# Kernel tuning notes

Hardware: AMD Instinct MI355X
Metric: run time of the kernel (lower is better)

## Reference

```python
import jax, jax.numpy as jnp
import numpy as np

GAMMA = 1.0
BIG = 1e10  # finite stand-in for +inf boundary; exp(-BIG) underflows to exactly 0 (grad-safe)


def setup_inputs() -> dict:
    key = jax.random.key(0)
    k1, k2 = jax.random.split(key)
    B, L, C = 64, 1024, 64
    x = jax.random.normal(k1, (B, L, C), dtype=jnp.float32)
    y = jax.random.normal(k2, (B, L, C), dtype=jnp.float32)
    return {"x": x, "y": y}


def _soft_dtw(x, y, gamma=GAMMA):
    B, L, C = x.shape
    # squared-euclidean pairwise cost, scaled by 1/gamma (matches torch code)
    x2 = jnp.sum(x * x, axis=-1)[:, :, None]            # [B,L,1]
    y2 = jnp.sum(y * y, axis=-1)[:, None, :]            # [B,1,L]
    D = (x2 + y2 - 2.0 * jnp.einsum('blc,bmc->blm', x, y)) / gamma  # [B,L,L]

    # Anti-diagonal wavefront DP over the (L+2)x(L+2) R matrix.
    # r_d[i] holds R[i, d-i] for the diagonal i+j=d, i in 0..L+1.
    n = L + 2
    ii = jnp.arange(n)
    i_idx = jnp.clip(ii - 1, 0, L - 1)
    r_prev2 = jnp.full((B, n), BIG, dtype=x.dtype).at[:, 0].set(0.0)  # diag d=0: R[0,0]=0
    r_prev1 = jnp.full((B, n), BIG, dtype=x.dtype)                    # diag d=1: all boundary
    big_col = jnp.full((B, 1), BIG, dtype=x.dtype)

    def step(carry, d):
        rp2, rp1 = carry
        jj = d - ii
        valid = (ii >= 1) & (ii <= L) & (jj >= 1) & (jj <= L)
        j_idx = jnp.clip(jj - 1, 0, L - 1)
        d_vals = D[:, i_idx, j_idx]                                   # [B,n] cost along diagonal
        r_diag = jnp.concatenate([big_col, rp2[:, :-1]], axis=1)      # R[i-1, j-1]
        r_up   = jnp.concatenate([big_col, rp1[:, :-1]], axis=1)      # R[i-1, j]
        r_left = rp1                                                  # R[i,   j-1]
        z = jnp.stack([-r_diag, -r_up, -r_left], axis=-1)             # [B,n,3]
        zmax = jnp.max(z, axis=-1)
        softmin = -(jnp.log(jnp.sum(jnp.exp(z - zmax[..., None]), axis=-1)) + zmax)
        new = jnp.where(valid[None, :], d_vals + softmin, BIG)
        return (rp1, new), None

    (_, r_last), _ = jax.lax.scan(step, (r_prev2, r_prev1), jnp.arange(2, 2 * L + 1))
    # last diagonal is d=2L; R[L,L] sits at index i=L
    return r_last[:, L] * gamma


def reference(x, y):
    return _soft_dtw(x, y)
```

## Files before the change

### kernel.cpp

```cpp
#include <hip/hip_runtime.h>


typedef unsigned short ushort_t;
typedef __attribute__((ext_vector_type(8))) short short8;
typedef __attribute__((ext_vector_type(4))) float f32x4;
typedef __attribute__((ext_vector_type(4))) unsigned short ushort4v;

constexpr int B_ = 64, L_ = 1024, C_ = 64;
constexpr int DSTR = 130;
constexpr int HBSTR = 1280;

#define BIGV 1e10f
#define INV_LN2 1.44269504088896340736f
#define LN2F 0.69314718055994530942f
#define DPP_WAVE_SHL1 0x130
#define DPP_WAVE_SHR1 0x138

static __device__ __forceinline__ ushort_t f2bf(float f) {
  unsigned u = __builtin_bit_cast(unsigned, f);
  unsigned r = (u + 0x7fffu + ((u >> 16) & 1u)) >> 16;
  return (ushort_t)r;
}
static __device__ __forceinline__ float exp2_(float x) {
  float r; asm("v_exp_f32 %0, %1" : "=v"(r) : "v"(x)); return r;
}
static __device__ __forceinline__ float log2_(float x) {
  float r; asm("v_log_f32 %0, %1" : "=v"(r) : "v"(x)); return r;
}
static __device__ __forceinline__ unsigned cvt_pk_bf16(float lo, float hi) {
  unsigned r; asm("v_cvt_pk_bf16_f32 %0, %1, %2" : "=v"(r) : "v"(lo), "v"(hi)); return r;
}
static __device__ __forceinline__ float dpp_shr1(float old, float src) {
  return __builtin_bit_cast(float, __builtin_amdgcn_update_dpp(
      __builtin_bit_cast(int, old), __builtin_bit_cast(int, src),
      DPP_WAVE_SHR1, 0xF, 0xF, false));
}
static __device__ __forceinline__ float dpp_shl1(float v) {
  return __builtin_bit_cast(float, __builtin_amdgcn_update_dpp(
      __builtin_bit_cast(int, v), __builtin_bit_cast(int, v),
      DPP_WAVE_SHL1, 0xF, 0xF, false));
}

__global__ __launch_bounds__(256) void prep_kernel(
    const float* __restrict__ x, const float* __restrict__ y,
    ushort_t* __restrict__ xb, ushort_t* __restrict__ yb,
    float* __restrict__ x2, float* __restrict__ y2, int* __restrict__ flagsG)
{
  if (blockIdx.x == 0 && threadIdx.x < 192) flagsG[threadIdx.x] = 0;
  const int lane = threadIdx.x & 63;
  const int sub = lane >> 4;
  const int cg  = lane & 15;
  const int wv = (blockIdx.x * blockDim.x + threadIdx.x) >> 6;
  const int nw = (gridDim.x * blockDim.x) >> 6;
  const int totalGroups = (2 * B_ * L_) >> 2;
  for (int g = wv; g < totalGroups; g += nw) {
    int r = g * 4 + sub;
    const float* src; ushort_t* dst; float* nrm;
    if (r < B_ * L_) { src = x; dst = xb; nrm = x2; }
    else             { r -= B_ * L_; src = y; dst = yb; nrm = y2; }
    const float4 v = *(const float4*)(src + (size_t)r * C_ + cg * 4);
    ushort4v p;
    p.x = f2bf(v.x); p.y = f2bf(v.y); p.z = f2bf(v.z); p.w = f2bf(v.w);
    *(ushort4v*)(dst + (size_t)r * C_ + cg * 4) = p;
    float s = v.x*v.x + v.y*v.y + v.z*v.z + v.w*v.w;
    s += __shfl_xor(s, 1); s += __shfl_xor(s, 2);
    s += __shfl_xor(s, 4); s += __shfl_xor(s, 8);
    if (cg == 0) nrm[r] = s * INV_LN2;
  }
}

template<int HDST, bool FIRST>
static __device__ __forceinline__ void dp_chunk(
    const int t, const int lane, float& cur, float& dgp, float hvv,
    const float zsel, const ushort_t* __restrict__ DtwLane,
    float* __restrict__ HbDst, float* __restrict__ HXB)
{
  const unsigned* pw = (const unsigned*)(DtwLane + ((t << 6) & 127));
  const int cb = (t << 6) - 63;
  unsigned a0 = pw[0], a1 = pw[1], b0 = pw[2], b1 = pw[3];

  auto step = [&](unsigned dw, int k, int u) -> float {
    float dv = __builtin_bit_cast(float, (k & 1) ? (dw & 0xffff0000u) : (dw << 16));
    float up = dpp_shr1(hvv, cur);
    float dg = dgp, lf = cur;
    if constexpr (FIRST) {
      bool at0 = (u == lane);
      dg = at0 ? zsel : dg;
      lf = at0 ? BIGV : lf;
    }
    float mn = fminf(fminf(up, dg), lf);
    float e = exp2_(mn - up) + exp2_(mn - dg) + exp2_(mn - lf);
    float nv = (dv + mn) - log2_(e);
    dgp = up;
    hvv = dpp_shl1(hvv);
    if constexpr (FIRST) { if (u >= lane) cur = nv; }
    else cur = nv;
    return nv;
  };
  auto flush4 = [&](int c0, float v0, float v1, float v2, float v3) {
    if constexpr (HDST == 0) {
      if (lane == 63) { HbDst[c0] = v0; HbDst[c0+1] = v1; HbDst[c0+2] = v2; HbDst[c0+3] = v3; }
    } else if constexpr (HDST == 1) {
      if (lane == 63) { HXB[c0] = v0; HXB[c0+1] = v1; HXB[c0+2] = v2; HXB[c0+3] = v3; }
    }
  };

  #pragma unroll 1
  for (int g = 0; g < 8; ++g) {
    const int u0 = g * 8;
    unsigned n0 = 0, n1 = 0, n2 = 0, n3 = 0;
    if (g < 7) {
      n0 = pw[u0/2 + 4]; n1 = pw[u0/2 + 5]; n2 = pw[u0/2 + 6]; n3 = pw[u0/2 + 7];
    }
    float v0 = step(a0, 0, u0 + 0);
    float v1 = step(a0, 1, u0 + 1);
    float v2 = step(a1, 0, u0 + 2);
    float v3 = step(a1, 1, u0 + 3);
    if constexpr (!FIRST) flush4(cb + u0, v0, v1, v2, v3);
    float v4 = step(b0, 0, u0 + 4);
    float v5 = step(b0, 1, u0 + 5);
    float v6 = step(b1, 0, u0 + 6);
    float v7 = step(b1, 1, u0 + 7);
    if constexpr (!FIRST) flush4(cb + u0 + 4, v4, v5, v6, v7);
    a0 = n0; a1 = n1; b0 = n2; b1 = n3;
    (void)v0; (void)v1; (void)v2; (void)v3; (void)v4; (void)v5; (void)v6; (void)v7;
  }
  if constexpr (FIRST) {
    if constexpr (HDST == 0) { if (lane == 63) HbDst[0] = cur; }
    else if constexpr (HDST == 1) { if (lane == 63) HXB[0] = cur; }
  }
}

template<int HDST>
static __device__ __forceinline__ void dp_tail(
    const int lane, float& cur, float& dgp,
    const ushort_t* __restrict__ DtwLane,
    float* __restrict__ HbDst, float* __restrict__ HXB)
{
  const unsigned* pw = (const unsigned*)(DtwLane);
  #pragma unroll 1
  for (int g = 0; g < 8; ++g) {
    unsigned w0 = pw[g*4], w1 = pw[g*4+1], w2 = pw[g*4+2], w3 = pw[g*4+3];
    #pragma unroll
    for (int k = 0; k < 8; ++k) {
      const int u = g * 8 + k;
      unsigned dw = (k < 2) ? w0 : (k < 4) ? w1 : (k < 6) ? w2 : w3;
      float dv = __builtin_bit_cast(float, (k & 1) ? (dw & 0xffff0000u) : (dw << 16));
      float up = dpp_shr1(BIGV, cur);
      float dg = dgp, lf = cur;
      float mn = fminf(fminf(up, dg), lf);
      float e = exp2_(mn - up) + exp2_(mn - dg) + exp2_(mn - lf);
      float nv = (dv + mn) - log2_(e);
      dgp = up;
      if (u < lane) {
        cur = nv;
        if constexpr (HDST == 0) { if (lane == 63) HbDst[961 + u] = nv; }
        else if constexpr (HDST == 1) { if (lane == 63) HXB[961 + u] = nv; }
      }
    }
  }
}

static __device__ __forceinline__ void spin_lds(int* f, int v) {
  int k = 0;
  while (__hip_atomic_load(f, __ATOMIC_ACQUIRE, __HIP_MEMORY_SCOPE_WORKGROUP) < v) {
    __builtin_amdgcn_s_sleep(1);
    if (++k > (1 << 26)) break;
  }
}
static __device__ __forceinline__ void spin_glb(int* f, int v) {
  int k = 0;
  while (__hip_atomic_load(f, __ATOMIC_ACQUIRE, __HIP_MEMORY_SCOPE_AGENT) < v) {
    __builtin_amdgcn_s_sleep(8);
    if (++k > (1 << 26)) break;
  }
}

template<int HSRC, int HDST>
static __device__ __forceinline__ void run_band(
    const ushort_t* __restrict__ xbB, const ushort_t* __restrict__ ybB,
    const float* __restrict__ x2B, const float* __restrict__ y2B,
    const float* __restrict__ HXin, float* __restrict__ HXout,
    int* __restrict__ fGin, int* __restrict__ fGout,
    ushort_t* __restrict__ Dtw, const float* __restrict__ HbSrc,
    float* __restrict__ HbDst, int* __restrict__ cin, int* __restrict__ cout,
    const int lane, const int W, float* __restrict__ outp)
{
  const int m = lane & 15, q = lane >> 4;
  const int i0 = W * 64;

  short8 af[4][2];
  #pragma unroll
  for (int mt = 0; mt < 4; ++mt)
    #pragma unroll
    for (int ks = 0; ks < 2; ++ks)
      af[mt][ks] = *(const short8*)(xbB + (size_t)(i0 + mt * 16 + m) * C_ + ks * 32 + q * 8);
  f32x4 x2q[4];
  #pragma unroll
  for (int mt = 0; mt < 4; ++mt) x2q[mt] = *(const f32x4*)(x2B + i0 + mt * 16 + q * 4);

  short8 bfr0[4], bfr1[4];
  auto load_bfr = [&](int tc) {
    const ushort_t* yb0 = ybB + (size_t)tc * 64 * C_;
    #pragma unroll
    for (int nt = 0; nt < 4; ++nt) {
      bfr0[nt] = *(const short8*)(yb0 + (size_t)(nt * 16 + m) * C_ + q * 8);
      bfr1[nt] = *(const short8*)(yb0 + (size_t)(nt * 16 + m) * C_ + 32 + q * 8);
    }
  };
  auto gram = [&](int tc) {
    const int cb = tc * 64;
    const float* y2j = y2B + cb;
    #pragma unroll
    for (int mt = 0; mt < 4; ++mt) {
      const int r0 = mt * 16 + q * 4;
      #pragma unroll
      for (int nt = 0; nt < 4; ++nt) {
        f32x4 acc = {0.f, 0.f, 0.f, 0.f};
        acc = __builtin_amdgcn_mfma_f32_16x16x32_bf16(af[mt][0], bfr0[nt], acc, 0, 0, 0);
        acc = __builtin_amdgcn_mfma_f32_16x16x32_bf16(af[mt][1], bfr1[nt], acc, 0, 0, 0);
        float y2v = y2j[nt * 16 + m];
        float d0 = fmaf(acc[0], -2.f * INV_LN2, x2q[mt][0] + y2v);
        float d1 = fmaf(acc[1], -2.f * INV_LN2, x2q[mt][1] + y2v);
        float d2 = fmaf(acc[2], -2.f * INV_LN2, x2q[mt][2] + y2v);
        float d3 = fmaf(acc[3], -2.f * INV_LN2, x2q[mt][3] + y2v);
        unsigned p01 = cvt_pk_bf16(d0, d1);
        unsigned p23 = cvt_pk_bf16(d2, d3);
        const int cs = cb + nt * 16 + m + r0;
        ushort_t* base = Dtw + r0 * DSTR;
        base[             ( cs      & 127)] = (ushort_t)p01;
        base[    DSTR  +  ((cs + 1) & 127)] = (ushort_t)(p01 >> 16);
        base[2 * DSTR  +  ((cs + 2) & 127)] = (ushort_t)p23;
        base[3 * DSTR  +  ((cs + 3) & 127)] = (ushort_t)(p23 >> 16);
      }
    }
  };

  float cur = 0.f, dgp = BIGV;
  const float zsel = (W == 0 && lane == 0) ? 0.f : BIGV;
  const ushort_t* DtwLane = Dtw + lane * DSTR;

  load_bfr(0);
  gram(0);

  #pragma unroll 1
  for (int t = 0; t < 16; ++t) {
    if (t < 15) load_bfr(t + 1);
    float hvv;
    if constexpr (HSRC == 0) {
      hvv = BIGV;
    } else if constexpr (HSRC == 1) {
      spin_lds(cin, t + 1);
      hvv = HbSrc[(t << 6) + lane];
    } else {
      spin_glb(fGin, t + 1);
      hvv = HXin[(t << 6) + lane];
    }
    if (t == 0) dp_chunk<HDST, true >(0, lane, cur, dgp, hvv, zsel, DtwLane, HbDst, HXout);
    else        dp_chunk<HDST, false>(t, lane, cur, dgp, hvv, zsel, DtwLane, HbDst, HXout);
    if constexpr (HDST == 0) {
      if (lane == 0) __hip_atomic_store(cout, t, __ATOMIC_RELEASE, __HIP_MEMORY_SCOPE_WORKGROUP);
    } else if constexpr (HDST == 1) {
      if (lane == 0) __hip_atomic_store(fGout, t, __ATOMIC_RELEASE, __HIP_MEMORY_SCOPE_AGENT);
    }
    if (t < 15) gram(t + 1);
  }
  dp_tail<HDST>(lane, cur, dgp, DtwLane, HbDst, HXout);
  if constexpr (HDST == 0) {
    if (lane == 0) __hip_atomic_store(cout, 16, __ATOMIC_RELEASE, __HIP_MEMORY_SCOPE_WORKGROUP);
  } else if constexpr (HDST == 1) {
    if (lane == 0) __hip_atomic_store(fGout, 16, __ATOMIC_RELEASE, __HIP_MEMORY_SCOPE_AGENT);
  }
  if (W == 15 && lane == 63) *outp = cur * LN2F;
}

__global__ __launch_bounds__(256) void sdtw_kernel(
    const ushort_t* __restrict__ xb, const ushort_t* __restrict__ yb,
    const float* __restrict__ x2g, const float* __restrict__ y2g,
    float* __restrict__ HXg, int* __restrict__ flagsG,
    float* __restrict__ out)
{
  __shared__ ushort_t Dt[4][64 * DSTR];
  __shared__ float Hb[3][HBSTR];
  __shared__ int cflag[4];

  const int b = blockIdx.x & 63;
  const int sub = blockIdx.x >> 6;
  const int w = threadIdx.x >> 6;
  const int lane = threadIdx.x & 63;
  const int W = sub * 4 + w;

  if (threadIdx.x < 4) cflag[threadIdx.x] = 0;
  __syncthreads();

  const ushort_t* xbB = xb + (size_t)b * L_ * C_;
  const ushort_t* ybB = yb + (size_t)b * L_ * C_;
  const float* x2B = x2g + b * L_;
  const float* y2B = y2g + b * L_;
  const float* HXin = HXg + ((size_t)b * 3 + (sub - 1)) * L_;
  float* HXout      = HXg + ((size_t)b * 3 + sub) * L_;
  int* fGin  = flagsG + b * 3 + (sub - 1);
  int* fGout = flagsG + b * 3 + sub;
  ushort_t* Dtw = &Dt[w][0];
  const float* HbSrc = (w > 0) ? &Hb[w - 1][0] : &Hb[0][0];
  float* HbDst = (w < 3) ? &Hb[w][0] : &Hb[0][0];
  int* cin  = (w > 0) ? &cflag[w - 1] : &cflag[0];
  int* cout = (w < 3) ? &cflag[w] : &cflag[3];
  float* outp = out + b;

  if (sub == 0) {
    if (w == 0)      run_band<0, 0>(xbB, ybB, x2B, y2B, HXin, HXout, fGin, fGout, Dtw, HbSrc, HbDst, cin, cout, lane, W, outp);
    else if (w < 3)  run_band<1, 0>(xbB, ybB, x2B, y2B, HXin, HXout, fGin, fGout, Dtw, HbSrc, HbDst, cin, cout, lane, W, outp);
    else             run_band<1, 1>(xbB, ybB, x2B, y2B, HXin, HXout, fGin, fGout, Dtw, HbSrc, HbDst, cin, cout, lane, W, outp);
  } else if (sub < 3) {
    if (w == 0)      run_band<2, 0>(xbB, ybB, x2B, y2B, HXin, HXout, fGin, fGout, Dtw, HbSrc, HbDst, cin, cout, lane, W, outp);
    else if (w < 3)  run_band<1, 0>(xbB, ybB, x2B, y2B, HXin, HXout, fGin, fGout, Dtw, HbSrc, HbDst, cin, cout, lane, W, outp);
    else             run_band<1, 1>(xbB, ybB, x2B, y2B, HXin, HXout, fGin, fGout, Dtw, HbSrc, HbDst, cin, cout, lane, W, outp);
  } else {
    if (w == 0)      run_band<2, 0>(xbB, ybB, x2B, y2B, HXin, HXout, fGin, fGout, Dtw, HbSrc, HbDst, cin, cout, lane, W, outp);
    else if (w < 3)  run_band<1, 0>(xbB, ybB, x2B, y2B, HXin, HXout, fGin, fGout, Dtw, HbSrc, HbDst, cin, cout, lane, W, outp);
    else             run_band<1, 2>(xbB, ybB, x2B, y2B, HXin, HXout, fGin, fGout, Dtw, HbSrc, HbDst, cin, cout, lane, W, outp);
  }
}

extern "C" void kernel_launch(void* const* d_in, const int* in_sizes, int n_in,
                              void* d_out, int out_size, void* d_ws, size_t ws_size,
                              hipStream_t stream) {
  const float* x = (const float*)d_in[0];
  const float* y = (const float*)d_in[1];
  float* out = (float*)d_out;

  char* ws = (char*)d_ws;
  const size_t XB = (size_t)B_ * L_ * C_ * 2;
  const size_t NB = (size_t)B_ * L_ * 4;
  ushort_t* xb = (ushort_t*)ws;
  ushort_t* yb = (ushort_t*)(ws + XB);
  float* x2 = (float*)(ws + 2 * XB);
  float* y2 = (float*)(ws + 2 * XB + NB);
  float* HX = (float*)(ws + 2 * XB + 2 * NB);
  int* flagsG = (int*)(ws + 2 * XB + 2 * NB + (size_t)B_ * 3 * L_ * 4);

  prep_kernel<<<512, 256, 0, stream>>>(x, y, xb, yb, x2, y2, flagsG);
  sdtw_kernel<<<256, 256, 0, stream>>>(xb, yb, x2, y2, HX, flagsG, out);
}
```

Before: 355.3 us.

## Give each wave two interleaved 64-row DP strips to halve blocks and chains

Each wave now owns 128 rows of the DP and runs two 64-row strips, A and B, as a skewed pair inside one dp_chunk. Strip B's upper neighbor comes from strip A through a DPP rotate, and the two softmin chains are interleaved for instruction-level parallelism. The grid shrinks from 256 to 128 blocks, so there are fewer cross-block global handoffs (one per batch instead of three), and the Gram tiles for both strips are software-pipelined. The trade-offs are a longer per-wave serial chain, more register pressure from 8 A-fragments, a larger LDS footprint, and fewer active CUs. The global spin sleep is also shortened.

New measurement: 392.0 us. +10.3%, slower.

```diff
diff --git a/kernel.cpp b/kernel.cpp
--- a/kernel.cpp
+++ b/kernel.cpp
@@ -8,37 +8,30 @@
 
 constexpr int B_ = 64, L_ = 1024, C_ = 64;
 constexpr int DSTR = 130;
-constexpr int HBSTR = 1280;
 
 #define BIGV 1e10f
 #define INV_LN2 1.44269504088896340736f
 #define LN2F 0.69314718055994530942f
-#define DPP_WAVE_SHL1 0x130
-#define DPP_WAVE_SHR1 0x138
 
 static __device__ __forceinline__ ushort_t f2bf(float f) {
   unsigned u = __builtin_bit_cast(unsigned, f);
   unsigned r = (u + 0x7fffu + ((u >> 16) & 1u)) >> 16;
   return (ushort_t)r;
 }
-static __device__ __forceinline__ float exp2_(float x) {
-  float r; asm("v_exp_f32 %0, %1" : "=v"(r) : "v"(x)); return r;
-}
-static __device__ __forceinline__ float log2_(float x) {
-  float r; asm("v_log_f32 %0, %1" : "=v"(r) : "v"(x)); return r;
-}
 static __device__ __forceinline__ unsigned cvt_pk_bf16(float lo, float hi) {
   unsigned r; asm("v_cvt_pk_bf16_f32 %0, %1, %2" : "=v"(r) : "v"(lo), "v"(hi)); return r;
 }
 static __device__ __forceinline__ float dpp_shr1(float old, float src) {
   return __builtin_bit_cast(float, __builtin_amdgcn_update_dpp(
-      __builtin_bit_cast(int, old), __builtin_bit_cast(int, src),
-      DPP_WAVE_SHR1, 0xF, 0xF, false));
+      __builtin_bit_cast(int, old), __builtin_bit_cast(int, src), 0x138, 0xF, 0xF, false));
 }
 static __device__ __forceinline__ float dpp_shl1(float v) {
   return __builtin_bit_cast(float, __builtin_amdgcn_update_dpp(
-      __builtin_bit_cast(int, v), __builtin_bit_cast(int, v),
-      DPP_WAVE_SHL1, 0xF, 0xF, false));
+      __builtin_bit_cast(int, v), __builtin_bit_cast(int, v), 0x130, 0xF, 0xF, false));
+}
+static __device__ __forceinline__ float dpp_ror1(float v) {
+  return __builtin_bit_cast(float, __builtin_amdgcn_update_dpp(
+      __builtin_bit_cast(int, v), __builtin_bit_cast(int, v), 0x13C, 0xF, 0xF, false));
 }
 
 __global__ __launch_bounds__(256) void prep_kernel(
@@ -46,7 +39,7 @@
     ushort_t* __restrict__ xb, ushort_t* __restrict__ yb,
     float* __restrict__ x2, float* __restrict__ y2, int* __restrict__ flagsG)
 {
-  if (blockIdx.x == 0 && threadIdx.x < 192) flagsG[threadIdx.x] = 0;
+  if (blockIdx.x == 0 && threadIdx.x < 64) flagsG[threadIdx.x] = 0;
   const int lane = threadIdx.x & 63;
   const int sub = lane >> 4;
   const int cg  = lane & 15;
@@ -69,94 +62,34 @@
   }
 }
 
-template<int HDST, bool FIRST>
-static __device__ __forceinline__ void dp_chunk(
-    const int t, const int lane, float& cur, float& dgp, float hvv,
-    const float zsel, const ushort_t* __restrict__ DtwLane,
-    float* __restrict__ HbDst, float* __restrict__ HXB)
-{
-  const unsigned* pw = (const unsigned*)(DtwLane + ((t << 6) & 127));
-  const int cb = (t << 6) - 63;
-  unsigned a0 = pw[0], a1 = pw[1], b0 = pw[2], b1 = pw[3];
-
-  auto step = [&](unsigned dw, int k, int u) -> float {
-    float dv = __builtin_bit_cast(float, (k & 1) ? (dw & 0xffff0000u) : (dw << 16));
-    float up = dpp_shr1(hvv, cur);
-    float dg = dgp, lf = cur;
-    if constexpr (FIRST) {
-      bool at0 = (u == lane);
-      dg = at0 ? zsel : dg;
-      lf = at0 ? BIGV : lf;
-    }
-    float mn = fminf(fminf(up, dg), lf);
-    float e = exp2_(mn - up) + exp2_(mn - dg) + exp2_(mn - lf);
-    float nv = (dv + mn) - log2_(e);
-    dgp = up;
-    hvv = dpp_shl1(hvv);
-    if constexpr (FIRST) { if (u >= lane) cur = nv; }
-    else cur = nv;
-    return nv;
-  };
-  auto flush4 = [&](int c0, float v0, float v1, float v2, float v3) {
-    if constexpr (HDST == 0) {
-      if (lane == 63) { HbDst[c0] = v0; HbDst[c0+1] = v1; HbDst[c0+2] = v2; HbDst[c0+3] = v3; }
-    } else if constexpr (HDST == 1) {
-      if (lane == 63) { HXB[c0] = v0; HXB[c0+1] = v1; HXB[c0+2] = v2; HXB[c0+3] = v3; }
-    }
-  };
-
-  #pragma unroll 1
-  for (int g = 0; g < 8; ++g) {
-    const int u0 = g * 8;
-    unsigned n0 = 0, n1 = 0, n2 = 0, n3 = 0;
-    if (g < 7) {
-      n0 = pw[u0/2 + 4]; n1 = pw[u0/2 + 5]; n2 = pw[u0/2 + 6]; n3 = pw[u0/2 + 7];
-    }
-    float v0 = step(a0, 0, u0 + 0);
-    float v1 = step(a0, 1, u0 + 1);
-    float v2 = step(a1, 0, u0 + 2);
-    float v3 = step(a1, 1, u0 + 3);
-    if constexpr (!FIRST) flush4(cb + u0, v0, v1, v2, v3);
-    float v4 = step(b0, 0, u0 + 4);
-    float v5 = step(b0, 1, u0 + 5);
-    float v6 = step(b1, 0, u0 + 6);
-    float v7 = step(b1, 1, u0 + 7);
-    if constexpr (!FIRST) flush4(cb + u0 + 4, v4, v5, v6, v7);
-    a0 = n0; a1 = n1; b0 = n2; b1 = n3;
-    (void)v0; (void)v1; (void)v2; (void)v3; (void)v4; (void)v5; (void)v6; (void)v7;
-  }
-  if constexpr (FIRST) {
-    if constexpr (HDST == 0) { if (lane == 63) HbDst[0] = cur; }
-    else if constexpr (HDST == 1) { if (lane == 63) HXB[0] = cur; }
-  }
-}
-
-template<int HDST>
-static __device__ __forceinline__ void dp_tail(
-    const int lane, float& cur, float& dgp,
-    const ushort_t* __restrict__ DtwLane,
-    float* __restrict__ HbDst, float* __restrict__ HXB)
-{
-  const unsigned* pw = (const unsigned*)(DtwLane);
-  #pragma unroll 1
-  for (int g = 0; g < 8; ++g) {
-    unsigned w0 = pw[g*4], w1 = pw[g*4+1], w2 = pw[g*4+2], w3 = pw[g*4+3];
-    #pragma unroll
-    for (int k = 0; k < 8; ++k) {
-      const int u = g * 8 + k;
-      unsigned dw = (k < 2) ? w0 : (k < 4) ? w1 : (k < 6) ? w2 : w3;
-      float dv = __builtin_bit_cast(float, (k & 1) ? (dw & 0xffff0000u) : (dw << 16));
-      float up = dpp_shr1(BIGV, cur);
-      float dg = dgp, lf = cur;
-      float mn = fminf(fminf(up, dg), lf);
-      float e = exp2_(mn - up) + exp2_(mn - dg) + exp2_(mn - lf);
-      float nv = (dv + mn) - log2_(e);
-      dgp = up;
-      if (u < lane) {
-        cur = nv;
-        if constexpr (HDST == 0) { if (lane == 63) HbDst[961 + u] = nv; }
-        else if constexpr (HDST == 1) { if (lane == 63) HXB[961 + u] = nv; }
-      }
+template<int MTB>
+static __device__ __forceinline__ void gram_tile(
+    const short8 (&af)[8][2], const f32x4 (&x2q)[8],
+    const short8 (&b0)[4], const short8 (&b1)[4], const f32x4 y2r,
+    ushort_t* __restrict__ Dtw, const int rowBase, const int cb,
+    const int m, const int q)
+{
+  #pragma unroll
+  for (int mt = 0; mt < 4; ++mt) {
+    const int r0 = mt * 16 + q * 4;
+    #pragma unroll
+    for (int nt = 0; nt < 4; ++nt) {
+      f32x4 acc = {0.f, 0.f, 0.f, 0.f};
+      acc = __builtin_amdgcn_mfma_f32_16x16x32_bf16(af[MTB + mt][0], b0[nt], acc, 0, 0, 0);
+      acc = __builtin_amdgcn_mfma_f32_16x16x32_bf16(af[MTB + mt][1], b1[nt], acc, 0, 0, 0);
+      const float y2v = y2r[nt];
+      float d0 = fmaf(acc[0], -2.f * INV_LN2, x2q[MTB + mt][0] + y2v);
+      float d1 = fmaf(acc[1], -2.f * INV_LN2, x2q[MTB + mt][1] + y2v);
+      float d2 = fmaf(acc[2], -2.f * INV_LN2, x2q[MTB + mt][2] + y2v);
+      float d3 = fmaf(acc[3], -2.f * INV_LN2, x2q[MTB + mt][3] + y2v);
+      unsigned p01 = cvt_pk_bf16(d0, d1);
+      unsigned p23 = cvt_pk_bf16(d2, d3);
+      const int cs = cb + nt * 16 + m + r0;
+      ushort_t* base = Dtw + (rowBase + r0) * DSTR;
+      base[             ((cs    ) & 127)] = (ushort_t)p01;
+      base[    DSTR  +  ((cs + 1) & 127)] = (ushort_t)(p01 >> 16);
+      base[2 * DSTR  +  ((cs + 2) & 127)] = (ushort_t)p23;
+      base[3 * DSTR  +  ((cs + 3) & 127)] = (ushort_t)(p23 >> 16);
     }
   }
 }
@@ -171,8 +104,121 @@
 static __device__ __forceinline__ void spin_glb(int* f, int v) {
   int k = 0;
   while (__hip_atomic_load(f, __ATOMIC_ACQUIRE, __HIP_MEMORY_SCOPE_AGENT) < v) {
-    __builtin_amdgcn_s_sleep(8);
+    __builtin_amdgcn_s_sleep(2);
     if (++k > (1 << 26)) break;
+  }
+}
+
+template<int HDST, int MODE>
+static __device__ __forceinline__ void dp_chunk(
+    const int t, const int lane,
+    float& curA, float& curB, float& dgpA, float& dgpB,
+    float hvv, const float zsel,
+    const unsigned* __restrict__ pwA, const unsigned* __restrict__ pwB,
+    float* __restrict__ HbDst, float* __restrict__ HXB)
+{
+  const int cb2 = (t << 6) - 127;
+  unsigned aA0=0,aA1=0,aA2=0,aA3=0,aB0=0,aB1=0,aB2=0,aB3=0;
+  if constexpr (MODE != 4) { aA0=pwA[0]; aA1=pwA[1]; aA2=pwA[2]; aA3=pwA[3]; }
+  if constexpr (MODE != 0) { aB0=pwB[0]; aB1=pwB[1]; aB2=pwB[2]; aB3=pwB[3]; }
+
+  auto step = [&](unsigned dwA, int kA, unsigned dwB, int kB, int u) -> float {
+    float rolA = dpp_ror1(curA);
+    float upA  = dpp_shr1(hvv, curA);
+    if constexpr (MODE != 4) {
+      float dvA = __builtin_bit_cast(float, (kA & 1) ? (dwA & 0xffff0000u) : (dwA << 16));
+      float dgA = dgpA, lfA = curA;
+      if constexpr (MODE == 0) {
+        const bool a0 = (u == lane);
+        dgA = a0 ? zsel : dgA;
+        lfA = a0 ? BIGV : lfA;
+      }
+      float mnA = fminf(fminf(upA, dgA), lfA);
+      float eA = __builtin_amdgcn_exp2f(mnA - upA) + __builtin_amdgcn_exp2f(mnA - dgA)
+               + __builtin_amdgcn_exp2f(mnA - lfA);
+      float nvA = (dvA + mnA) - __builtin_amdgcn_logf(eA);
+      if constexpr (MODE == 0)      { if (u >= lane) curA = nvA; }
+      else if constexpr (MODE == 3) { if (u <  lane) curA = nvA; }
+      else                          curA = nvA;
+    }
+    dgpA = upA;
+    hvv = dpp_shl1(hvv);
+    float nvB = 0.f;
+    if constexpr (MODE != 0) {
+      float upB = dpp_shr1(rolA, curB);
+      float dvB = __builtin_bit_cast(float, (kB & 1) ? (dwB & 0xffff0000u) : (dwB << 16));
+      float dgB = dgpB, lfB = curB;
+      if constexpr (MODE == 1) {
+        const bool b0c = (u == lane);
+        dgB = b0c ? BIGV : dgB;
+        lfB = b0c ? BIGV : lfB;
+      }
+      float mnB = fminf(fminf(upB, dgB), lfB);
+      float eB = __builtin_amdgcn_exp2f(mnB - upB) + __builtin_amdgcn_exp2f(mnB - dgB)
+               + __builtin_amdgcn_exp2f(mnB - lfB);
+      nvB = (dvB + mnB) - __builtin_amdgcn_logf(eB);
+      dgpB = upB;
+      if constexpr (MODE == 1) {
+        if (u >= lane) {
+          curB = nvB;
+          if (lane == 63) {
+            if constexpr (HDST == 0) HbDst[0] = nvB;
+            else if constexpr (HDST == 1) HXB[0] = nvB;
+          }
+        }
+      } else if constexpr (MODE == 4) {
+        if (u < lane) {
+          curB = nvB;
+          if (lane == 63) {
+            if constexpr (HDST == 0) HbDst[961 + u] = nvB;
+            else if constexpr (HDST == 1) HXB[961 + u] = nvB;
+          }
+        }
+      } else {
+        curB = nvB;
+      }
+    }
+    return nvB;
+  };
+
+  #pragma unroll 1
+  for (int g = 0; g < 8; ++g) {
+    unsigned nA0=0,nA1=0,nA2=0,nA3=0,nB0=0,nB1=0,nB2=0,nB3=0;
+    if (g < 7) {
+      const int o = (g + 1) * 4;
+      if constexpr (MODE != 4) { nA0=pwA[o]; nA1=pwA[o+1]; nA2=pwA[o+2]; nA3=pwA[o+3]; }
+      if constexpr (MODE != 0) { nB0=pwB[o]; nB1=pwB[o+1]; nB2=pwB[o+2]; nB3=pwB[o+3]; }
+    }
+    const int u0 = g << 3;
+    float v0 = step(aA0,0,aB0,0,u0+0);
+    float v1 = step(aA0,1,aB0,1,u0+1);
+    float v2 = step(aA1,0,aB1,0,u0+2);
+    float v3 = step(aA1,1,aB1,1,u0+3);
+    if constexpr (MODE == 2 || MODE == 3) {
+      if (lane == 63) {
+        if constexpr (HDST == 0) {
+          HbDst[cb2+u0]=v0; HbDst[cb2+u0+1]=v1; HbDst[cb2+u0+2]=v2; HbDst[cb2+u0+3]=v3;
+        } else if constexpr (HDST == 1) {
+          HXB[cb2+u0]=v0; HXB[cb2+u0+1]=v1; HXB[cb2+u0+2]=v2; HXB[cb2+u0+3]=v3;
+        }
+      }
+    }
+    float v4 = step(aA2,0,aB2,0,u0+4);
+    float v5 = step(aA2,1,aB2,1,u0+5);
+    float v6 = step(aA3,0,aB3,0,u0+6);
+    float v7 = step(aA3,1,aB3,1,u0+7);
+    if constexpr (MODE == 2 || MODE == 3) {
+      if (lane == 63) {
+        if constexpr (HDST == 0) {
+          HbDst[cb2+u0+4]=v4; HbDst[cb2+u0+5]=v5; HbDst[cb2+u0+6]=v6; HbDst[cb2+u0+7]=v7;
+        } else if constexpr (HDST == 1) {
+          HXB[cb2+u0+4]=v4; HXB[cb2+u0+5]=v5; HXB[cb2+u0+6]=v6; HXB[cb2+u0+7]=v7;
+        }
+      }
+    }
+    aA0=nA0; aA1=nA1; aA2=nA2; aA3=nA3;
+    aB0=nB0; aB1=nB1; aB2=nB2; aB3=nB3;
+    (void)v0;(void)v1;(void)v2;(void)v3;(void)v4;(void)v5;(void)v6;(void)v7;
   }
 }
 
@@ -187,91 +233,96 @@
     const int lane, const int W, float* __restrict__ outp)
 {
   const int m = lane & 15, q = lane >> 4;
-  const int i0 = W * 64;
-
-  short8 af[4][2];
+  const int i0 = W * 128;
+
+  short8 af[8][2];
   #pragma unroll
-  for (int mt = 0; mt < 4; ++mt)
+  for (int mt = 0; mt < 8; ++mt)
     #pragma unroll
     for (int ks = 0; ks < 2; ++ks)
       af[mt][ks] = *(const short8*)(xbB + (size_t)(i0 + mt * 16 + m) * C_ + ks * 32 + q * 8);
-  f32x4 x2q[4];
+  f32x4 x2q[8];
   #pragma unroll
-  for (int mt = 0; mt < 4; ++mt) x2q[mt] = *(const f32x4*)(x2B + i0 + mt * 16 + q * 4);
-
-  short8 bfr0[4], bfr1[4];
-  auto load_bfr = [&](int tc) {
+  for (int mt = 0; mt < 8; ++mt) x2q[mt] = *(const f32x4*)(x2B + i0 + mt * 16 + q * 4);
+
+  short8 bc0[4], bc1[4], bn0[4], bn1[4];
+  f32x4 y2c = {0.f,0.f,0.f,0.f}, y2n = {0.f,0.f,0.f,0.f};
+  auto load_y = [&](int tc, short8 (&b0)[4], short8 (&b1)[4], f32x4& y2r) {
     const ushort_t* yb0 = ybB + (size_t)tc * 64 * C_;
     #pragma unroll
     for (int nt = 0; nt < 4; ++nt) {
-      bfr0[nt] = *(const short8*)(yb0 + (size_t)(nt * 16 + m) * C_ + q * 8);
-      bfr1[nt] = *(const short8*)(yb0 + (size_t)(nt * 16 + m) * C_ + 32 + q * 8);
-    }
-  };
-  auto gram = [&](int tc) {
-    const int cb = tc * 64;
-    const float* y2j = y2B + cb;
-    #pragma unroll
-    for (int mt = 0; mt < 4; ++mt) {
-      const int r0 = mt * 16 + q * 4;
-      #pragma unroll
-      for (int nt = 0; nt < 4; ++nt) {
-        f32x4 acc = {0.f, 0.f, 0.f, 0.f};
-        acc = __builtin_amdgcn_mfma_f32_16x16x32_bf16(af[mt][0], bfr0[nt], acc, 0, 0, 0);
-        acc = __builtin_amdgcn_mfma_f32_16x16x32_bf16(af[mt][1], bfr1[nt], acc, 0, 0, 0);
-        float y2v = y2j[nt * 16 + m];
-        float d0 = fmaf(acc[0], -2.f * INV_LN2, x2q[mt][0] + y2v);
-        float d1 = fmaf(acc[1], -2.f * INV_LN2, x2q[mt][1] + y2v);
-        float d2 = fmaf(acc[2], -2.f * INV_LN2, x2q[mt][2] + y2v);
-        float d3 = fmaf(acc[3], -2.f * INV_LN2, x2q[mt][3] + y2v);
-        unsigned p01 = cvt_pk_bf16(d0, d1);
-        unsigned p23 = cvt_pk_bf16(d2, d3);
-        const int cs = cb + nt * 16 + m + r0;
-        ushort_t* base = Dtw + r0 * DSTR;
-        base[             ( cs      & 127)] = (ushort_t)p01;
-        base[    DSTR  +  ((cs + 1) & 127)] = (ushort_t)(p01 >> 16);
-        base[2 * DSTR  +  ((cs + 2) & 127)] = (ushort_t)p23;
-        base[3 * DSTR  +  ((cs + 3) & 127)] = (ushort_t)(p23 >> 16);
-      }
-    }
-  };
-
-  float cur = 0.f, dgp = BIGV;
+      b0[nt] = *(const short8*)(yb0 + (size_t)(nt * 16 + m) * C_ + q * 8);
+      b1[nt] = *(const short8*)(yb0 + (size_t)(nt * 16 + m) * C_ + 32 + q * 8);
+    }
+    const float* y2j = y2B + tc * 64;
+    #pragma unroll
+    for (int nt = 0; nt < 4; ++nt) y2r[nt] = y2j[nt * 16 + m];
+  };
+  auto rot = [&]() {
+    #pragma unroll
+    for (int nt = 0; nt < 4; ++nt) { bc0[nt] = bn0[nt]; bc1[nt] = bn1[nt]; }
+    y2c = y2n;
+  };
+  auto get_hvv = [&](int t) -> float {
+    if constexpr (HSRC == 0) return BIGV;
+    else if constexpr (HSRC == 1) { spin_lds(cin, t + 1); return HbSrc[(t << 6) + lane]; }
+    else { spin_glb(fGin, t + 1); return HXin[(t << 6) + lane]; }
+  };
+  auto signal = [&](int v) {
+    if constexpr (HDST == 0) {
+      if (lane == 0) __hip_atomic_store(cout, v, __ATOMIC_RELEASE, __HIP_MEMORY_SCOPE_WORKGROUP);
+    } else if constexpr (HDST == 1) {
+      if (lane == 0) __hip_atomic_store(fGout, v, __ATOMIC_RELEASE, __HIP_MEMORY_SCOPE_AGENT);
+    }
+  };
+
+  float curA = 0.f, curB = 0.f, dgpA = BIGV, dgpB = BIGV;
   const float zsel = (W == 0 && lane == 0) ? 0.f : BIGV;
-  const ushort_t* DtwLane = Dtw + lane * DSTR;
-
-  load_bfr(0);
-  gram(0);
+  const unsigned* DtU = (const unsigned*)Dtw;
+  const unsigned* pA = DtU + lane * (DSTR / 2);
+  const unsigned* pB = DtU + (64 + lane) * (DSTR / 2);
+
+  load_y(0, bc0, bc1, y2c);
+  gram_tile<0>(af, x2q, bc0, bc1, y2c, Dtw, 0, 0, m, q);
+
+  load_y(1, bn0, bn1, y2n);
+  { float hv = get_hvv(0);
+    dp_chunk<HDST, 0>(0, lane, curA, curB, dgpA, dgpB, hv, zsel, pA, pB, HbDst, HXout); }
+  gram_tile<0>(af, x2q, bn0, bn1, y2n, Dtw, 0, 64, m, q);
+  gram_tile<4>(af, x2q, bc0, bc1, y2c, Dtw, 64, 0, m, q);
+  rot();
+
+  load_y(2, bn0, bn1, y2n);
+  { float hv = get_hvv(1);
+    dp_chunk<HDST, 1>(1, lane, curA, curB, dgpA, dgpB, hv, zsel, pA + 32, pB, HbDst, HXout); }
+  gram_tile<0>(af, x2q, bn0, bn1, y2n, Dtw, 0, 128, m, q);
+  gram_tile<4>(af, x2q, bc0, bc1, y2c, Dtw, 64, 64, m, q);
+  rot();
 
   #pragma unroll 1
-  for (int t = 0; t < 16; ++t) {
-    if (t < 15) load_bfr(t + 1);
-    float hvv;
-    if constexpr (HSRC == 0) {
-      hvv = BIGV;
-    } else if constexpr (HSRC == 1) {
-      spin_lds(cin, t + 1);
-      hvv = HbSrc[(t << 6) + lane];
-    } else {
-      spin_glb(fGin, t + 1);
-      hvv = HXin[(t << 6) + lane];
-    }
-    if (t == 0) dp_chunk<HDST, true >(0, lane, cur, dgp, hvv, zsel, DtwLane, HbDst, HXout);
-    else        dp_chunk<HDST, false>(t, lane, cur, dgp, hvv, zsel, DtwLane, HbDst, HXout);
-    if constexpr (HDST == 0) {
-      if (lane == 0) __hip_atomic_store(cout, t, __ATOMIC_RELEASE, __HIP_MEMORY_SCOPE_WORKGROUP);
-    } else if constexpr (HDST == 1) {
-      if (lane == 0) __hip_atomic_store(fGout, t, __ATOMIC_RELEASE, __HIP_MEMORY_SCOPE_AGENT);
-    }
-    if (t < 15) gram(t + 1);
-  }
-  dp_tail<HDST>(lane, cur, dgp, DtwLane, HbDst, HXout);
-  if constexpr (HDST == 0) {
-    if (lane == 0) __hip_atomic_store(cout, 16, __ATOMIC_RELEASE, __HIP_MEMORY_SCOPE_WORKGROUP);
-  } else if constexpr (HDST == 1) {
-    if (lane == 0) __hip_atomic_store(fGout, 16, __ATOMIC_RELEASE, __HIP_MEMORY_SCOPE_AGENT);
-  }
-  if (W == 15 && lane == 63) *outp = cur * LN2F;
+  for (int t = 2; t <= 14; ++t) {
+    load_y(t + 1, bn0, bn1, y2n);
+    float hv = get_hvv(t);
+    dp_chunk<HDST, 2>(t, lane, curA, curB, dgpA, dgpB, hv, zsel,
+                      pA + ((t & 1) << 5), pB + (((t & 1) ^ 1) << 5), HbDst, HXout);
+    signal(t - 1);
+    gram_tile<0>(af, x2q, bn0, bn1, y2n, Dtw, 0, (t + 1) << 6, m, q);
+    gram_tile<4>(af, x2q, bc0, bc1, y2c, Dtw, 64, t << 6, m, q);
+    rot();
+  }
+
+  { float hv = get_hvv(15);
+    dp_chunk<HDST, 2>(15, lane, curA, curB, dgpA, dgpB, hv, zsel, pA + 32, pB, HbDst, HXout);
+    signal(14);
+    gram_tile<4>(af, x2q, bc0, bc1, y2c, Dtw, 64, 15 << 6, m, q); }
+
+  dp_chunk<HDST, 3>(16, lane, curA, curB, dgpA, dgpB, BIGV, zsel, pA, pB + 32, HbDst, HXout);
+  signal(15);
+
+  dp_chunk<HDST, 4>(17, lane, curA, curB, dgpA, dgpB, BIGV, zsel, pA + 32, pB, HbDst, HXout);
+  signal(16);
+
+  if (W == 7 && lane == 63) *outp = curB * LN2F;
 }
 
 __global__ __launch_bounds__(256) void sdtw_kernel(
@@ -280,15 +331,15 @@
     float* __restrict__ HXg, int* __restrict__ flagsG,
     float* __restrict__ out)
 {
-  __shared__ ushort_t Dt[4][64 * DSTR];
-  __shared__ float Hb[3][HBSTR];
+  __shared__ ushort_t Dt[4][128 * DSTR];
+  __shared__ float Hb[3][1024];
   __shared__ int cflag[4];
 
   const int b = blockIdx.x & 63;
-  const int sub = blockIdx.x >> 6;
+  const int half = blockIdx.x >> 6;
   const int w = threadIdx.x >> 6;
   const int lane = threadIdx.x & 63;
-  const int W = sub * 4 + w;
+  const int W = half * 4 + w;
 
   if (threadIdx.x < 4) cflag[threadIdx.x] = 0;
   __syncthreads();
@@ -297,10 +348,10 @@
   const ushort_t* ybB = yb + (size_t)b * L_ * C_;
   const float* x2B = x2g + b * L_;
   const float* y2B = y2g + b * L_;
-  const float* HXin = HXg + ((size_t)b * 3 + (sub - 1)) * L_;
-  float* HXout      = HXg + ((size_t)b * 3 + sub) * L_;
-  int* fGin  = flagsG + b * 3 + (sub - 1);
-  int* fGout = flagsG + b * 3 + sub;
+  const float* HXin = HXg + (size_t)b * L_;
+  float* HXout     = HXg + (size_t)b * L_;
+  int* fGin  = flagsG + b;
+  int* fGout = flagsG + b;
   ushort_t* Dtw = &Dt[w][0];
   const float* HbSrc = (w > 0) ? &Hb[w - 1][0] : &Hb[0][0];
   float* HbDst = (w < 3) ? &Hb[w][0] : &Hb[0][0];
@@ -308,18 +359,20 @@
   int* cout = (w < 3) ? &cflag[w] : &cflag[3];
   float* outp = out + b;
 
-  if (sub == 0) {
-    if (w == 0)      run_band<0, 0>(xbB, ybB, x2B, y2B, HXin, HXout, fGin, fGout, Dtw, HbSrc, HbDst, cin, cout, lane, W, outp);
-    else if (w < 3)  run_band<1, 0>(xbB, ybB, x2B, y2B, HXin, HXout, fGin, fGout, Dtw, HbSrc, HbDst, cin, cout, lane, W, outp);
-    else             run_band<1, 1>(xbB, ybB, x2B, y2B, HXin, HXout, fGin, fGout, Dtw, HbSrc, HbDst, cin, cout, lane, W, outp);
-  } else if (sub < 3) {
-    if (w == 0)      run_band<2, 0>(xbB, ybB, x2B, y2B, HXin, HXout, fGin, fGout, Dtw, HbSrc, HbDst, cin, cout, lane, W, outp);
-    else if (w < 3)  run_band<1, 0>(xbB, ybB, x2B, y2B, HXin, HXout, fGin, fGout, Dtw, HbSrc, HbDst, cin, cout, lane, W, outp);
-    else             run_band<1, 1>(xbB, ybB, x2B, y2B, HXin, HXout, fGin, fGout, Dtw, HbSrc, HbDst, cin, cout, lane, W, outp);
+  if (half == 0) {
+    if (w == 0)
+      run_band<0, 0>(xbB, ybB, x2B, y2B, HXin, HXout, fGin, fGout, Dtw, HbSrc, HbDst, cin, cout, lane, W, outp);
+    else if (w < 3)
+      run_band<1, 0>(xbB, ybB, x2B, y2B, HXin, HXout, fGin, fGout, Dtw, HbSrc, HbDst, cin, cout, lane, W, outp);
+    else
+      run_band<1, 1>(xbB, ybB, x2B, y2B, HXin, HXout, fGin, fGout, Dtw, HbSrc, HbDst, cin, cout, lane, W, outp);
   } else {
-    if (w == 0)      run_band<2, 0>(xbB, ybB, x2B, y2B, HXin, HXout, fGin, fGout, Dtw, HbSrc, HbDst, cin, cout, lane, W, outp);
-    else if (w < 3)  run_band<1, 0>(xbB, ybB, x2B, y2B, HXin, HXout, fGin, fGout, Dtw, HbSrc, HbDst, cin, cout, lane, W, outp);
-    else             run_band<1, 2>(xbB, ybB, x2B, y2B, HXin, HXout, fGin, fGout, Dtw, HbSrc, HbDst, cin, cout, lane, W, outp);
+    if (w == 0)
+      run_band<2, 0>(xbB, ybB, x2B, y2B, HXin, HXout, fGin, fGout, Dtw, HbSrc, HbDst, cin, cout, lane, W, outp);
+    else if (w < 3)
+      run_band<1, 0>(xbB, ybB, x2B, y2B, HXin, HXout, fGin, fGout, Dtw, HbSrc, HbDst, cin, cout, lane, W, outp);
+    else
+      run_band<1, 2>(xbB, ybB, x2B, y2B, HXin, HXout, fGin, fGout, Dtw, HbSrc, HbDst, cin, cout, lane, W, outp);
   }
 }
 
@@ -338,8 +391,8 @@
   float* x2 = (float*)(ws + 2 * XB);
   float* y2 = (float*)(ws + 2 * XB + NB);
   float* HX = (float*)(ws + 2 * XB + 2 * NB);
-  int* flagsG = (int*)(ws + 2 * XB + 2 * NB + (size_t)B_ * 3 * L_ * 4);
+  int* flagsG = (int*)(ws + 2 * XB + 3 * NB);
 
   prep_kernel<<<512, 256, 0, stream>>>(x, y, xb, yb, x2, y2, flagsG);
-  sdtw_kernel<<<256, 256, 0, stream>>>(xb, yb, x2, y2, HX, flagsG, out);
-}
+  sdtw_kernel<<<128, 256, 0, stream>>>(xb, yb, x2, y2, HX, flagsG, out);
+}
```
